# Kernel optimization log

Measured on AMD Instinct MI355X. Metric: run time of the kernel, lower is better.

The kernel has to match this reference:

```python
import jax, jax.numpy as jnp
import numpy as np
import math

D_MODEL = 1024
N_HEADS = 16
HEAD_DIM = D_MODEL // N_HEADS


def setup_inputs() -> dict:
    key = jax.random.key(0)
    k1, k2, k3 = jax.random.split(key, 3)
    B, T = 2, 2048
    x = jax.random.normal(k1, (B, T, D_MODEL), dtype=jnp.float32)
    W_qkv = jax.random.normal(k2, (D_MODEL, 3 * D_MODEL), dtype=jnp.float32) * (1.0 / math.sqrt(D_MODEL))
    W_out = jax.random.normal(k3, (D_MODEL, D_MODEL), dtype=jnp.float32) * (1.0 / math.sqrt(D_MODEL))
    return {"x": x, "W_qkv": W_qkv, "W_out": W_out}


def reference(x, W_qkv, W_out):
    B, T, C = x.shape
    qkv = x @ W_qkv  # [B, T, 3C]
    q, k, v = jnp.split(qkv, 3, axis=-1)

    def heads(t):  # [B,T,C] -> [B,H,T,Dh]
        return t.reshape(B, T, N_HEADS, HEAD_DIM).transpose(0, 2, 1, 3)

    q, k, v = heads(q), heads(k), heads(v)
    scale = 1.0 / math.sqrt(HEAD_DIM)
    scores = jnp.einsum('bhtd,bhsd->bhts', q, k) * scale  # [B,H,T,T]
    causal = jnp.tril(jnp.ones((T, T), dtype=bool))
    scores = jnp.where(causal[None, None, :, :], scores, -jnp.inf)
    attn = jax.nn.softmax(scores, axis=-1)
    out = jnp.einsum('bhts,bhsd->bhtd', attn, v)  # [B,H,T,Dh]
    out = out.transpose(0, 2, 1, 3).reshape(B, T, C)
    return out @ W_out
```

## Files before the change

kernel.cpp:

```cpp
#include <hip/hip_runtime.h>
#include <hip/hip_bf16.h>

typedef __bf16 bf16;
typedef bf16 bf16x4 __attribute__((ext_vector_type(4)));
typedef bf16 bf16x8 __attribute__((ext_vector_type(8)));
typedef float f32x4 __attribute__((ext_vector_type(4)));

#define GLOAD16(g, l) __builtin_amdgcn_global_load_lds( \
    (const __attribute__((address_space(1))) void*)(g),  \
    (__attribute__((address_space(3))) void*)(l), 16, 0, 0)

#define EXP2F(x) __builtin_amdgcn_exp2f(x)
#define MFMA16(a, b, c) __builtin_amdgcn_mfma_f32_16x16x32_bf16(a, b, c, 0, 0, 0)

__global__ __launch_bounds__(256) void prep(const float* __restrict__ x,
                                            const float* __restrict__ Wqkv,
                                            const float* __restrict__ Wout,
                                            bf16* __restrict__ xb,
                                            bf16* __restrict__ wqkvT,
                                            bf16* __restrict__ woutT) {
  int id = blockIdx.x, tid = threadIdx.x;
  if (id < 2048) {
    int i = id * 256 + tid;
    const float4* p = (const float4*)x + (size_t)i * 2;
    float4 a = p[0], b = p[1];
    bf16x8 o;
    o[0] = (bf16)a.x; o[1] = (bf16)a.y; o[2] = (bf16)a.z; o[3] = (bf16)a.w;
    o[4] = (bf16)b.x; o[5] = (bf16)b.y; o[6] = (bf16)b.z; o[7] = (bf16)b.w;
    ((bf16x8*)xb)[i] = o;
  } else {
    __shared__ float tile[32][33];
    const float* src; bf16* dst; int N, j;
    if (id < 5120) { src = Wqkv; dst = wqkvT; N = 3072; j = id - 2048; }
    else           { src = Wout; dst = woutT; N = 1024; j = id - 5120; }
    int ntile = N / 32;
    int n0 = (j % ntile) * 32, k0 = (j / ntile) * 32;
    int tx = tid & 31, ty = tid >> 5;
#pragma unroll
    for (int i = 0; i < 4; i++)
      tile[ty + 8 * i][tx] = src[(size_t)(k0 + ty + 8 * i) * N + n0 + tx];
    __syncthreads();
#pragma unroll
    for (int i = 0; i < 4; i++)
      dst[(size_t)(n0 + ty + 8 * i) * 1024 + k0 + tx] = (bf16)tile[tx][ty + 8 * i];
  }
}

__device__ __forceinline__ void gemm_mainloop64(const bf16* __restrict__ A,
                                                const bf16* __restrict__ Bt,
                                                int K, int m0, int n0,
                                                f32x4 acc[4][4],
                                                bf16* As, bf16* Bs) {
  int tid = threadIdx.x;
  int lane = tid & 63;
  int wave = tid >> 6;
  int wr = wave >> 1, wc = wave & 1;
  int c16 = lane & 15, g = lane >> 4;
  f32x4 z = {0.f, 0.f, 0.f, 0.f};
#pragma unroll
  for (int m = 0; m < 4; m++)
#pragma unroll
    for (int n = 0; n < 4; n++) acc[m][n] = z;
  for (int k0 = 0; k0 < K; k0 += 64) {
#pragma unroll
    for (int i = 0; i < 4; i++) {
      int cc = tid + i * 256;
      int r = cc >> 3, ch = cc & 7;
      int sc = ch ^ (r & 7);
      GLOAD16(A + (size_t)(m0 + r) * K + k0 + sc * 8, As + cc * 8);
    }
#pragma unroll
    for (int i = 0; i < 4; i++) {
      int cc = tid + i * 256;
      int r = cc >> 3, ch = cc & 7;
      int sc = ch ^ (r & 7);
      GLOAD16(Bt + (size_t)(n0 + r) * K + k0 + sc * 8, Bs + cc * 8);
    }
    __syncthreads();
#pragma unroll
    for (int h = 0; h < 2; h++) {
      bf16x8 af[4], bfr[4];
#pragma unroll
      for (int m = 0; m < 4; m++) {
        int ar = wr * 64 + m * 16 + c16;
        af[m] = *(const bf16x8*)((const char*)As + ar * 128 + (((h * 4 + g) ^ (ar & 7)) << 4));
      }
#pragma unroll
      for (int n = 0; n < 4; n++) {
        int br = wc * 64 + n * 16 + c16;
        bfr[n] = *(const bf16x8*)((const char*)Bs + br * 128 + (((h * 4 + g) ^ (br & 7)) << 4));
      }
      __builtin_amdgcn_s_setprio(1);
#pragma unroll
      for (int m = 0; m < 4; m++)
#pragma unroll
        for (int n = 0; n < 4; n++)
          acc[m][n] = MFMA16(af[m], bfr[n], acc[m][n]);
      __builtin_amdgcn_s_setprio(0);
    }
    __syncthreads();
  }
}

__global__ __launch_bounds__(256) void gemm_qkv(const bf16* __restrict__ A,
                                                const bf16* __restrict__ Bt,
                                                bf16* __restrict__ q,
                                                bf16* __restrict__ kk,
                                                bf16* __restrict__ vt) {
  __shared__ bf16 As[128 * 64];
  __shared__ bf16 Bs[128 * 64];
  int id = blockIdx.x;
  int xc = id & 7, k = id >> 3;
  int bn = xc * 3 + (k % 3), bm = k / 3;
  int m0 = bm * 128, n0 = bn * 128;
  f32x4 acc[4][4];
  gemm_mainloop64(A, Bt, 1024, m0, n0, acc, As, Bs);
  int lane = threadIdx.x & 63;
  int wave = threadIdx.x >> 6;
  int wr = wave >> 1, wc = wave & 1;
  int c16 = lane & 15, g = lane >> 4;
  int which = n0 >> 10;
  const float QSCALE = 0.125f * 1.4426950408889634f;
  if (which == 2) {
#pragma unroll
    for (int m = 0; m < 4; m++)
#pragma unroll
      for (int n = 0; n < 4; n++) {
        int gm0 = m0 + wr * 64 + m * 16 + g * 4;
        int gn = n0 + wc * 64 + n * 16 + c16;
        int rem = gn & 1023, h = rem >> 6, d = rem & 63;
        int b = gm0 >> 11, t0 = gm0 & 2047;
        size_t bh = (size_t)(b * 16 + h);
        bf16x4 pv;
        pv[0] = (bf16)acc[m][n][0]; pv[1] = (bf16)acc[m][n][1];
        pv[2] = (bf16)acc[m][n][2]; pv[3] = (bf16)acc[m][n][3];
        *(bf16x4*)(vt + (bh * 64 + d) * 2048 + t0) = pv;
      }
  } else {
#pragma unroll
    for (int m = 0; m < 4; m++)
#pragma unroll
      for (int n = 0; n < 4; n++)
#pragma unroll
        for (int j = 0; j < 4; j++) {
          int gm = m0 + wr * 64 + m * 16 + g * 4 + j;
          int gn = n0 + wc * 64 + n * 16 + c16;
          int rem = gn & 1023, h = rem >> 6, d = rem & 63;
          int b = gm >> 11, t = gm & 2047;
          float v = acc[m][n][j];
          size_t bh = (size_t)(b * 16 + h);
          if (which == 0) q[(bh * 2048 + t) * 64 + d]  = (bf16)(v * QSCALE);
          else            kk[(bh * 2048 + t) * 64 + d] = (bf16)v;
        }
  }
}

__global__ __launch_bounds__(256) void gemm_out(const bf16* __restrict__ A,
                                                const bf16* __restrict__ Bt,
                                                float* __restrict__ C) {
  __shared__ bf16 As[128 * 64];
  __shared__ bf16 Bs[128 * 64];
  int id = blockIdx.x;
  int bn = id & 7, bm = id >> 3;
  int m0 = bm * 128, n0 = bn * 128;
  f32x4 acc[4][4];
  gemm_mainloop64(A, Bt, 1024, m0, n0, acc, As, Bs);
  int lane = threadIdx.x & 63;
  int wave = threadIdx.x >> 6;
  int wr = wave >> 1, wc = wave & 1;
#pragma unroll
  for (int m = 0; m < 4; m++)
#pragma unroll
    for (int n = 0; n < 4; n++)
#pragma unroll
      for (int j = 0; j < 4; j++) {
        int gm = m0 + wr * 64 + m * 16 + (lane >> 4) * 4 + j;
        int gn = n0 + wc * 64 + n * 16 + (lane & 15);
        C[(size_t)gm * 1024 + gn] = acc[m][n][j];
      }
}

__global__ __launch_bounds__(512) void attn(const bf16* __restrict__ q,
                                            const bf16* __restrict__ kk,
                                            const bf16* __restrict__ vt,
                                            bf16* __restrict__ out) {
  __shared__ bf16 Ks[4][64 * 64];
  __shared__ bf16 Vs[4][64 * 64];
  __shared__ bf16 Ps[8 * 16 * 64];
  int tid = threadIdx.x, lane = tid & 63, w = tid >> 6;
  int c16 = lane & 15, g = (lane >> 4) & 3, g4 = g * 4;

  int id = blockIdx.x;
  int c = id & 7;
  int k = id >> 3;
  int s = k >> 5;
  int j5 = k & 31;
  int bxi = j5 & 15, b2 = j5 >> 4;
  int bx = s ? (15 - bxi) : bxi;
  int bh = 4 * c + 2 * b2 + s;
  int q0 = bx * 128;

  const bf16* qb = q  + (size_t)bh * 2048 * 64;
  const bf16* kb = kk + (size_t)bh * 2048 * 64;
  const bf16* vb = vt + (size_t)bh * 64 * 2048;
  int nt = 2 * bx + 2;
  int ns = nt >> 1;

  int qlo = q0 + w * 16;
  int qr = qlo + c16;
  bf16x8 qf[2];
#pragma unroll
  for (int ks = 0; ks < 2; ks++)
    qf[ks] = *(const bf16x8*)(qb + (size_t)(qlo + c16) * 64 + ks * 32 + g * 8);
  int r = tid >> 3;
  int swz = ((tid & 7) ^ (r & 7)) * 8;
  GLOAD16(kb + (size_t)r * 64 + swz, Ks[0] + tid * 8);
  GLOAD16(vb + (size_t)r * 2048 + swz, Vs[0] + tid * 8);
  GLOAD16(kb + (size_t)(64 + r) * 64 + swz, Ks[1] + tid * 8);
  GLOAD16(vb + (size_t)r * 2048 + 64 + swz, Vs[1] + tid * 8);
  __syncthreads();

  f32x4 o[4];
  float mrun = -__builtin_inff(), lrun = 0.f;
  {
    f32x4 z = {0.f, 0.f, 0.f, 0.f};
#pragma unroll
    for (int n = 0; n < 4; n++) o[n] = z;
  }
  bf16* Pw = Ps + w * 1024;

  for (int st = 0; st < ns; ++st) {
    if (st + 1 < ns) {
      int sn = st * 128 + 128;
      int nb = (2 * st + 2) & 3;
      GLOAD16(kb + (size_t)(sn + r) * 64 + swz, Ks[nb] + tid * 8);
      GLOAD16(vb + (size_t)r * 2048 + sn + swz, Vs[nb] + tid * 8);
      GLOAD16(kb + (size_t)(sn + 64 + r) * 64 + swz, Ks[nb + 1] + tid * 8);
      GLOAD16(vb + (size_t)r * 2048 + sn + 64 + swz, Vs[nb + 1] + tid * 8);
    }
#pragma unroll
    for (int half = 0; half < 2; ++half) {
      int t = 2 * st + half;
      int s0 = t * 64;
      int cbuf = t & 3;
      if (s0 <= qlo + 15) {
        f32x4 S[4];
        {
          f32x4 z = {0.f, 0.f, 0.f, 0.f};
#pragma unroll
          for (int n = 0; n < 4; n++) S[n] = z;
        }
        __builtin_amdgcn_s_setprio(1);
#pragma unroll
        for (int ks = 0; ks < 2; ks++) {
          bf16x8 kf[4];
#pragma unroll
          for (int n = 0; n < 4; n++) {
            int srow = n * 16 + c16;
            kf[n] = *(const bf16x8*)((const char*)Ks[cbuf] + srow * 128 +
                                     (((ks * 4 + g) ^ (srow & 7)) << 4));
          }
#pragma unroll
          for (int n = 0; n < 4; n++)
            S[n] = MFMA16(kf[n], qf[ks], S[n]);
        }
        __builtin_amdgcn_s_setprio(0);
        if (s0 + 63 > qlo) {
#pragma unroll
          for (int n = 0; n < 4; n++)
#pragma unroll
            for (int rr = 0; rr < 4; rr++)
              if (s0 + n * 16 + g4 + rr > qr) S[n][rr] = -__builtin_inff();
        }
        float tm = fmaxf(fmaxf(fmaxf(S[0][0], S[0][1]), fmaxf(S[0][2], S[0][3])),
                         fmaxf(fmaxf(S[1][0], S[1][1]), fmaxf(S[1][2], S[1][3])));
        tm = fmaxf(tm, fmaxf(fmaxf(fmaxf(S[2][0], S[2][1]), fmaxf(S[2][2], S[2][3])),
                             fmaxf(fmaxf(S[3][0], S[3][1]), fmaxf(S[3][2], S[3][3]))));
        tm = fmaxf(tm, __shfl_xor(tm, 16));
        tm = fmaxf(tm, __shfl_xor(tm, 32));
        if (!__all(tm <= mrun + 8.f)) {
          float mnew = fmaxf(mrun, tm);
          float corr = EXP2F(mrun - mnew);
          lrun *= corr;
          mrun = mnew;
#pragma unroll
          for (int j = 0; j < 4; j++) {
            float cj = __shfl(corr, (lane & 48) | (g4 + j));
#pragma unroll
            for (int n = 0; n < 4; n++) o[n][j] *= cj;
          }
        }
        float p[4][4];
        float rs = 0.f;
#pragma unroll
        for (int n = 0; n < 4; n++)
#pragma unroll
          for (int rr = 0; rr < 4; rr++) {
            p[n][rr] = EXP2F(S[n][rr] - mrun);
            rs += p[n][rr];
          }
        rs += __shfl_xor(rs, 16);
        rs += __shfl_xor(rs, 32);
        lrun += rs;
#pragma unroll
        for (int n = 0; n < 4; n++) {
          bf16x4 pw;
          pw[0] = (bf16)p[n][0]; pw[1] = (bf16)p[n][1];
          pw[2] = (bf16)p[n][2]; pw[3] = (bf16)p[n][3];
          *(bf16x4*)(Pw + c16 * 64 + (((2 * n + (g >> 1)) ^ (c16 & 7)) * 8) + (g & 1) * 4) = pw;
        }
        __builtin_amdgcn_s_setprio(1);
#pragma unroll
        for (int ks = 0; ks < 2; ks++) {
          bf16x8 vf[4];
#pragma unroll
          for (int n = 0; n < 4; n++) {
            int drow = n * 16 + c16;
            vf[n] = *(const bf16x8*)((const char*)Vs[cbuf] + drow * 128 +
                                     (((ks * 4 + g) ^ (drow & 7)) << 4));
          }
          bf16x8 pf = *(const bf16x8*)(Pw + c16 * 64 + (((ks * 4 + g) ^ (c16 & 7)) * 8));
#pragma unroll
          for (int n = 0; n < 4; n++)
            o[n] = MFMA16(pf, vf[n], o[n]);
        }
        __builtin_amdgcn_s_setprio(0);
      }
    }
    if (st + 1 < ns) {
      asm volatile("s_waitcnt vmcnt(0)" ::: "memory");
      __builtin_amdgcn_s_barrier();
      __builtin_amdgcn_sched_barrier(0);
    }
  }
  int b = bh >> 4, h = bh & 15;
#pragma unroll
  for (int j = 0; j < 4; j++) {
    float lv = __shfl(lrun, (lane & 48) | (g4 + j));
    float inv = 1.f / lv;
    int t = qlo + g4 + j;
#pragma unroll
    for (int n = 0; n < 4; n++) {
      int col = h * 64 + n * 16 + c16;
      out[((size_t)(b * 2048 + t)) * 1024 + col] = (bf16)(o[n][j] * inv);
    }
  }
}

extern "C" void kernel_launch(void* const* d_in, const int* in_sizes, int n_in,
                              void* d_out, int out_size, void* d_ws, size_t ws_size,
                              hipStream_t stream) {
  const float* x    = (const float*)d_in[0];
  const float* Wqkv = (const float*)d_in[1];
  const float* Wout = (const float*)d_in[2];
  float* outp = (float*)d_out;
  char* ws = (char*)d_ws;
  const size_t MB = 1024 * 1024;
  bf16* xb    = (bf16*)(ws);
  bf16* wqkvT = (bf16*)(ws + 8 * MB);
  bf16* woutT = (bf16*)(ws + 14 * MB);
  bf16* qb    = (bf16*)(ws + 16 * MB);
  bf16* kb    = (bf16*)(ws + 24 * MB);
  bf16* vtb   = (bf16*)(ws + 32 * MB);

  hipLaunchKernelGGL(prep, dim3(6144), dim3(256), 0, stream,
                     x, Wqkv, Wout, xb, wqkvT, woutT);
  hipLaunchKernelGGL(gemm_qkv, dim3(768), dim3(256), 0, stream,
                     xb, wqkvT, qb, kb, vtb);
  hipLaunchKernelGGL(attn, dim3(512), dim3(512), 0, stream,
                     qb, kb, vtb, xb);
  hipLaunchKernelGGL(gemm_out, dim3(256), dim3(256), 0, stream,
                     xb, woutT, outp);
}
```

Measured before the change: 110.4 us.

## Issue both QK^T tiles before softmax in attention; halve gemm_out M tile

In the attention loop, the two 64-key halves of each stage now run their QK^T MFMAs back to back before either softmax/PV. This gives the scheduler independent MFMA work to overlap with the softmax math. Separately, gemm_out uses a dedicated 64x128 tile with its own single-buffered main loop and a 512-block grid, replacing the shared 128x128 mainloop. This raises block count for better CU occupancy, at the cost of more B-tile reloads and extra registers for the second S array.

```diff
diff --git a/kernel.cpp b/kernel.cpp
--- a/kernel.cpp
+++ b/kernel.cpp
@@ -158,24 +158,72 @@
 __global__ __launch_bounds__(256) void gemm_out(const bf16* __restrict__ A,
                                                 const bf16* __restrict__ Bt,
                                                 float* __restrict__ C) {
-  __shared__ bf16 As[128 * 64];
+  __shared__ bf16 As[64 * 64];
   __shared__ bf16 Bs[128 * 64];
+  int tid = threadIdx.x;
+  int lane = tid & 63;
+  int wave = tid >> 6;
+  int wr = wave >> 1, wc = wave & 1;
+  int c16 = lane & 15, g = lane >> 4;
   int id = blockIdx.x;
   int bn = id & 7, bm = id >> 3;
-  int m0 = bm * 128, n0 = bn * 128;
-  f32x4 acc[4][4];
-  gemm_mainloop64(A, Bt, 1024, m0, n0, acc, As, Bs);
-  int lane = threadIdx.x & 63;
-  int wave = threadIdx.x >> 6;
-  int wr = wave >> 1, wc = wave & 1;
-#pragma unroll
-  for (int m = 0; m < 4; m++)
+  int m0 = bm * 64, n0 = bn * 128;
+  const int K = 1024;
+  f32x4 acc[2][4];
+  {
+    f32x4 z = {0.f, 0.f, 0.f, 0.f};
+#pragma unroll
+    for (int m = 0; m < 2; m++)
+#pragma unroll
+      for (int n = 0; n < 4; n++) acc[m][n] = z;
+  }
+  for (int k0 = 0; k0 < K; k0 += 64) {
+#pragma unroll
+    for (int i = 0; i < 2; i++) {
+      int cc = tid + i * 256;
+      int r = cc >> 3, ch = cc & 7;
+      int sc = ch ^ (r & 7);
+      GLOAD16(A + (size_t)(m0 + r) * K + k0 + sc * 8, As + cc * 8);
+    }
+#pragma unroll
+    for (int i = 0; i < 4; i++) {
+      int cc = tid + i * 256;
+      int r = cc >> 3, ch = cc & 7;
+      int sc = ch ^ (r & 7);
+      GLOAD16(Bt + (size_t)(n0 + r) * K + k0 + sc * 8, Bs + cc * 8);
+    }
+    __syncthreads();
+#pragma unroll
+    for (int h = 0; h < 2; h++) {
+      bf16x8 af[2], bfr[4];
+#pragma unroll
+      for (int m = 0; m < 2; m++) {
+        int ar = wr * 32 + m * 16 + c16;
+        af[m] = *(const bf16x8*)((const char*)As + ar * 128 + (((h * 4 + g) ^ (ar & 7)) << 4));
+      }
+#pragma unroll
+      for (int n = 0; n < 4; n++) {
+        int br = wc * 64 + n * 16 + c16;
+        bfr[n] = *(const bf16x8*)((const char*)Bs + br * 128 + (((h * 4 + g) ^ (br & 7)) << 4));
+      }
+      __builtin_amdgcn_s_setprio(1);
+#pragma unroll
+      for (int m = 0; m < 2; m++)
+#pragma unroll
+        for (int n = 0; n < 4; n++)
+          acc[m][n] = MFMA16(af[m], bfr[n], acc[m][n]);
+      __builtin_amdgcn_s_setprio(0);
+    }
+    __syncthreads();
+  }
+#pragma unroll
+  for (int m = 0; m < 2; m++)
 #pragma unroll
     for (int n = 0; n < 4; n++)
 #pragma unroll
       for (int j = 0; j < 4; j++) {
-        int gm = m0 + wr * 64 + m * 16 + (lane >> 4) * 4 + j;
-        int gn = n0 + wc * 64 + n * 16 + (lane & 15);
+        int gm = m0 + wr * 32 + m * 16 + g * 4 + j;
+        int gn = n0 + wc * 64 + n * 16 + c16;
         C[(size_t)gm * 1024 + gn] = acc[m][n][j];
       }
 }
@@ -229,6 +277,89 @@
   }
   bf16* Pw = Ps + w * 1024;
 
+  auto QKT = [&](f32x4 S[4], const char* Kb) {
+    {
+      f32x4 z = {0.f, 0.f, 0.f, 0.f};
+#pragma unroll
+      for (int n = 0; n < 4; n++) S[n] = z;
+    }
+    __builtin_amdgcn_s_setprio(1);
+#pragma unroll
+    for (int ks = 0; ks < 2; ks++) {
+      bf16x8 kf[4];
+#pragma unroll
+      for (int n = 0; n < 4; n++) {
+        int srow = n * 16 + c16;
+        kf[n] = *(const bf16x8*)(Kb + srow * 128 + (((ks * 4 + g) ^ (srow & 7)) << 4));
+      }
+#pragma unroll
+      for (int n = 0; n < 4; n++)
+        S[n] = MFMA16(kf[n], qf[ks], S[n]);
+    }
+    __builtin_amdgcn_s_setprio(0);
+  };
+  auto SMPV = [&](f32x4 S[4], int s0, const char* Vb) {
+    if (s0 + 63 > qlo) {
+#pragma unroll
+      for (int n = 0; n < 4; n++)
+#pragma unroll
+        for (int rr = 0; rr < 4; rr++)
+          if (s0 + n * 16 + g4 + rr > qr) S[n][rr] = -__builtin_inff();
+    }
+    float tm = fmaxf(fmaxf(fmaxf(S[0][0], S[0][1]), fmaxf(S[0][2], S[0][3])),
+                     fmaxf(fmaxf(S[1][0], S[1][1]), fmaxf(S[1][2], S[1][3])));
+    tm = fmaxf(tm, fmaxf(fmaxf(fmaxf(S[2][0], S[2][1]), fmaxf(S[2][2], S[2][3])),
+                         fmaxf(fmaxf(S[3][0], S[3][1]), fmaxf(S[3][2], S[3][3]))));
+    tm = fmaxf(tm, __shfl_xor(tm, 16));
+    tm = fmaxf(tm, __shfl_xor(tm, 32));
+    if (!__all(tm <= mrun + 8.f)) {
+      float mnew = fmaxf(mrun, tm);
+      float corr = EXP2F(mrun - mnew);
+      lrun *= corr;
+      mrun = mnew;
+#pragma unroll
+      for (int j = 0; j < 4; j++) {
+        float cj = __shfl(corr, (lane & 48) | (g4 + j));
+#pragma unroll
+        for (int n = 0; n < 4; n++) o[n][j] *= cj;
+      }
+    }
+    float p[4][4];
+    float rs = 0.f;
+#pragma unroll
+    for (int n = 0; n < 4; n++)
+#pragma unroll
+      for (int rr = 0; rr < 4; rr++) {
+        p[n][rr] = EXP2F(S[n][rr] - mrun);
+        rs += p[n][rr];
+      }
+    rs += __shfl_xor(rs, 16);
+    rs += __shfl_xor(rs, 32);
+    lrun += rs;
+#pragma unroll
+    for (int n = 0; n < 4; n++) {
+      bf16x4 pw;
+      pw[0] = (bf16)p[n][0]; pw[1] = (bf16)p[n][1];
+      pw[2] = (bf16)p[n][2]; pw[3] = (bf16)p[n][3];
+      *(bf16x4*)(Pw + c16 * 64 + (((2 * n + (g >> 1)) ^ (c16 & 7)) * 8) + (g & 1) * 4) = pw;
+    }
+    __builtin_amdgcn_s_setprio(1);
+#pragma unroll
+    for (int ks = 0; ks < 2; ks++) {
+      bf16x8 vf[4];
+#pragma unroll
+      for (int n = 0; n < 4; n++) {
+        int drow = n * 16 + c16;
+        vf[n] = *(const bf16x8*)(Vb + drow * 128 + (((ks * 4 + g) ^ (drow & 7)) << 4));
+      }
+      bf16x8 pf = *(const bf16x8*)(Pw + c16 * 64 + (((ks * 4 + g) ^ (c16 & 7)) * 8));
+#pragma unroll
+      for (int n = 0; n < 4; n++)
+        o[n] = MFMA16(pf, vf[n], o[n]);
+    }
+    __builtin_amdgcn_s_setprio(0);
+  };
+
   for (int st = 0; st < ns; ++st) {
     if (st + 1 < ns) {
       int sn = st * 128 + 128;
@@ -238,95 +369,14 @@
       GLOAD16(kb + (size_t)(sn + 64 + r) * 64 + swz, Ks[nb + 1] + tid * 8);
       GLOAD16(vb + (size_t)r * 2048 + sn + 64 + swz, Vs[nb + 1] + tid * 8);
     }
-#pragma unroll
-    for (int half = 0; half < 2; ++half) {
-      int t = 2 * st + half;
-      int s0 = t * 64;
-      int cbuf = t & 3;
-      if (s0 <= qlo + 15) {
-        f32x4 S[4];
-        {
-          f32x4 z = {0.f, 0.f, 0.f, 0.f};
-#pragma unroll
-          for (int n = 0; n < 4; n++) S[n] = z;
-        }
-        __builtin_amdgcn_s_setprio(1);
-#pragma unroll
-        for (int ks = 0; ks < 2; ks++) {
-          bf16x8 kf[4];
-#pragma unroll
-          for (int n = 0; n < 4; n++) {
-            int srow = n * 16 + c16;
-            kf[n] = *(const bf16x8*)((const char*)Ks[cbuf] + srow * 128 +
-                                     (((ks * 4 + g) ^ (srow & 7)) << 4));
-          }
-#pragma unroll
-          for (int n = 0; n < 4; n++)
-            S[n] = MFMA16(kf[n], qf[ks], S[n]);
-        }
-        __builtin_amdgcn_s_setprio(0);
-        if (s0 + 63 > qlo) {
-#pragma unroll
-          for (int n = 0; n < 4; n++)
-#pragma unroll
-            for (int rr = 0; rr < 4; rr++)
-              if (s0 + n * 16 + g4 + rr > qr) S[n][rr] = -__builtin_inff();
-        }
-        float tm = fmaxf(fmaxf(fmaxf(S[0][0], S[0][1]), fmaxf(S[0][2], S[0][3])),
-                         fmaxf(fmaxf(S[1][0], S[1][1]), fmaxf(S[1][2], S[1][3])));
-        tm = fmaxf(tm, fmaxf(fmaxf(fmaxf(S[2][0], S[2][1]), fmaxf(S[2][2], S[2][3])),
-                             fmaxf(fmaxf(S[3][0], S[3][1]), fmaxf(S[3][2], S[3][3]))));
-        tm = fmaxf(tm, __shfl_xor(tm, 16));
-        tm = fmaxf(tm, __shfl_xor(tm, 32));
-        if (!__all(tm <= mrun + 8.f)) {
-          float mnew = fmaxf(mrun, tm);
-          float corr = EXP2F(mrun - mnew);
-          lrun *= corr;
-          mrun = mnew;
-#pragma unroll
-          for (int j = 0; j < 4; j++) {
-            float cj = __shfl(corr, (lane & 48) | (g4 + j));
-#pragma unroll
-            for (int n = 0; n < 4; n++) o[n][j] *= cj;
-          }
-        }
-        float p[4][4];
-        float rs = 0.f;
-#pragma unroll
-        for (int n = 0; n < 4; n++)
-#pragma unroll
-          for (int rr = 0; rr < 4; rr++) {
-            p[n][rr] = EXP2F(S[n][rr] - mrun);
-            rs += p[n][rr];
-          }
-        rs += __shfl_xor(rs, 16);
-        rs += __shfl_xor(rs, 32);
-        lrun += rs;
-#pragma unroll
-        for (int n = 0; n < 4; n++) {
-          bf16x4 pw;
-          pw[0] = (bf16)p[n][0]; pw[1] = (bf16)p[n][1];
-          pw[2] = (bf16)p[n][2]; pw[3] = (bf16)p[n][3];
-          *(bf16x4*)(Pw + c16 * 64 + (((2 * n + (g >> 1)) ^ (c16 & 7)) * 8) + (g & 1) * 4) = pw;
-        }
-        __builtin_amdgcn_s_setprio(1);
-#pragma unroll
-        for (int ks = 0; ks < 2; ks++) {
-          bf16x8 vf[4];
-#pragma unroll
-          for (int n = 0; n < 4; n++) {
-            int drow = n * 16 + c16;
-            vf[n] = *(const bf16x8*)((const char*)Vs[cbuf] + drow * 128 +
-                                     (((ks * 4 + g) ^ (drow & 7)) << 4));
-          }
-          bf16x8 pf = *(const bf16x8*)(Pw + c16 * 64 + (((ks * 4 + g) ^ (c16 & 7)) * 8));
-#pragma unroll
-          for (int n = 0; n < 4; n++)
-            o[n] = MFMA16(pf, vf[n], o[n]);
-        }
-        __builtin_amdgcn_s_setprio(0);
-      }
-    }
+    int t0 = 2 * st, t1 = 2 * st + 1;
+    int s00 = t0 * 64, s01 = t1 * 64;
+    bool c0 = (s00 <= qlo + 15), c1 = (s01 <= qlo + 15);
+    f32x4 S0[4], S1[4];
+    if (c0) QKT(S0, (const char*)Ks[t0 & 3]);
+    if (c1) QKT(S1, (const char*)Ks[t1 & 3]);
+    if (c0) SMPV(S0, s00, (const char*)Vs[t0 & 3]);
+    if (c1) SMPV(S1, s01, (const char*)Vs[t1 & 3]);
     if (st + 1 < ns) {
       asm volatile("s_waitcnt vmcnt(0)" ::: "memory");
       __builtin_amdgcn_s_barrier();
@@ -369,6 +419,6 @@
                      xb, wqkvT, qb, kb, vtb);
   hipLaunchKernelGGL(attn, dim3(512), dim3(512), 0, stream,
                      qb, kb, vtb, xb);
-  hipLaunchKernelGGL(gemm_out, dim3(256), dim3(256), 0, stream,
+  hipLaunchKernelGGL(gemm_out, dim3(512), dim3(256), 0, stream,
                      xb, woutT, outp);
 }
```

New measurement: 103.6 us (median of 2 runs). 6.2% less time.
